# Kernel tuning notes

Hardware: AMD Instinct MI355X
Metric: run time of the kernel (lower is better)

The kernel has to match this reference:

```python
import jax, jax.numpy as jnp
import numpy as np

K = 3
THRESHOLD = 0.05
RADIUS = 0.1
MIN_CORR = 3
MAX_CORR = 1500
N_ITER = 5
EPS = 1e-5
P, N = 1024, 128


def setup_inputs() -> dict:
    key = jax.random.key(0)
    k1, k2, k3, k4, k5 = jax.random.split(key, 5)
    # local knn patches: small spatial extent so matching_radius=0.1 is meaningful
    ref_knn_points = jax.random.normal(k1, (P, N, 3), jnp.float32) * 0.05
    src_knn_points = jax.random.normal(k2, (P, N, 3), jnp.float32) * 0.05
    ref_knn_masks = jax.random.uniform(k3, (P, N)) > 0.1
    src_knn_masks = jax.random.uniform(k4, (P, N)) > 0.1
    matching_score_map = jax.random.normal(k5, (P, N, N), jnp.float32)
    return {
        'ref_knn_points': ref_knn_points,
        'src_knn_points': src_knn_points,
        'ref_knn_masks': ref_knn_masks,
        'src_knn_masks': src_knn_masks,
        'matching_score_map': matching_score_map,
    }


def _kabsch(H, src_c, ref_c, bad):
    # guard degenerate (all-zero-weight) problems with a fixed full-rank H
    safe = jnp.diag(jnp.asarray([3.0, 2.0, 1.0], H.dtype))
    H = jnp.where(bad[..., None, None], safe, H)
    U, S, Vt = jnp.linalg.svd(H)
    V = jnp.swapaxes(Vt, -1, -2)
    Ut = jnp.swapaxes(U, -1, -2)
    det = jnp.linalg.det(V @ Ut)
    D = jnp.zeros_like(H).at[..., 0, 0].set(1.0).at[..., 1, 1].set(1.0).at[..., 2, 2].set(det)
    R = V @ D @ Ut
    t = ref_c - jnp.einsum('...cd,...d->...c', R, src_c)
    T = jnp.zeros(H.shape[:-2] + (4, 4), H.dtype)
    return T.at[..., :3, :3].set(R).at[..., :3, 3].set(t).at[..., 3, 3].set(1.0)


def pair_procrustes(src, ref, w):
    # src, ref: (..., M, 3); w: (..., M)
    tot = jnp.sum(w, -1, keepdims=True)
    wn = w / (tot + EPS)
    src_c = jnp.einsum('...m,...mc->...c', wn, src)
    ref_c = jnp.einsum('...m,...mc->...c', wn, ref)
    H = jnp.einsum('...mc,...m,...md->...cd', src - src_c[..., None, :], wn, ref - ref_c[..., None, :])
    return _kabsch(H, src_c, ref_c, tot[..., 0] < EPS)


def grid_procrustes(src, ref, W):
    # per-proposal weighted Procrustes over the full (ref_i, src_j) pair grid;
    # identical math to gathering nonzero pairs since zero-weight pairs drop out
    tot = jnp.sum(W, (1, 2))  # (P,)
    Wn = W / (tot[:, None, None] + EPS)
    ref_c = jnp.einsum('pij,pic->pc', Wn, ref)
    src_c = jnp.einsum('pij,pjc->pc', Wn, src)
    H = jnp.einsum('pjc,pij,pid->pcd', src - src_c[:, None], Wn, ref - ref_c[:, None])
    return _kabsch(H, src_c, ref_c, tot < EPS)


def _forward(ref_knn_points, src_knn_points, ref_knn_masks, src_knn_masks, matching_score_map):
    Pn, Nn, _ = matching_score_map.shape
    sm = jnp.exp(matching_score_map)
    corr_mask = ref_knn_masks[:, :, None] & src_knn_masks[:, None, :]

    pidx = jnp.arange(Pn)[:, None, None]
    lidx = jnp.arange(Nn)[None, :, None]
    # topk over src dim -> ref_score_map
    ref_ts, ref_ti = jax.lax.top_k(sm, K)
    ref_score_map = jnp.zeros_like(sm).at[pidx, lidx, ref_ti].set(ref_ts)
    # topk over ref dim -> src_score_map (via transpose)
    smT = jnp.swapaxes(sm, 1, 2)
    src_ts, src_ti = jax.lax.top_k(smT, K)
    src_score_map = jnp.swapaxes(jnp.zeros_like(smT).at[pidx, lidx, src_ti].set(src_ts), 1, 2)

    ref_corr = (ref_score_map > THRESHOLD) & corr_mask
    src_corr = (src_score_map > THRESHOLD) & corr_mask
    score_map = 0.5 * (ref_score_map + src_score_map)
    corr_map = ref_corr & src_corr

    # per-proposal Procrustes with pair-grid weights (zero weight = not a corr)
    W = jnp.where(corr_map, score_map, 0.0)
    counts = jnp.sum(corr_map, (1, 2))
    valid = counts >= MIN_CORR
    transforms = grid_procrustes(src_knn_points, ref_knn_points, W)  # (P,4,4)

    # global capped correspondence pool (top MAX_CORR by score)
    flat = jnp.where(corr_map, score_map, -1.0).reshape(-1)
    top_scores, top_flat = jax.lax.top_k(flat, MAX_CORR)
    p = top_flat // (Nn * Nn)
    rem = top_flat % (Nn * Nn)
    i = rem // Nn
    j = rem % Nn
    real = top_scores > 0.0  # padded slots if fewer than MAX_CORR corrs
    corr_scores = jnp.where(real, top_scores, 0.0)
    ref_pts = ref_knn_points[p, i]   # (M,3)
    src_pts = src_knn_points[p, j]   # (M,3)
    # padded candidates pushed far away so they are never inliers
    src_eval = src_pts + jnp.where(real, 0.0, 1e6)[:, None]

    # evaluate every proposal transform on the capped pool, pick max-inlier
    aligned = jnp.einsum('pcd,md->pmc', transforms[:, :3, :3], src_eval) + transforms[:, None, :3, 3]
    d2 = jnp.sum((ref_pts[None] - aligned) ** 2, -1)  # (P,M)
    inliers = d2 < RADIUS ** 2
    icount = jnp.where(valid, jnp.sum(inliers, 1), -1)
    best = jnp.argmax(icount)

    cur = corr_scores * inliers[best].astype(corr_scores.dtype)
    T = pair_procrustes(src_pts, ref_pts, cur)
    for _ in range(N_ITER - 1):
        al = src_eval @ T[:3, :3].T + T[:3, 3]
        d2 = jnp.sum((ref_pts - al) ** 2, -1)
        cur = corr_scores * (d2 < RADIUS ** 2).astype(corr_scores.dtype)
        T = pair_procrustes(src_pts, ref_pts, cur)

    return ref_pts, src_pts, corr_scores, T


def reference(ref_knn_points, src_knn_points, ref_knn_masks, src_knn_masks, matching_score_map):
    return _forward(ref_knn_points, src_knn_points, ref_knn_masks, src_knn_masks, matching_score_map)
```

## Files before the change

kernel.cpp:

```cpp
#include <hip/hip_runtime.h>
#include <math.h>

#define PP    1024
#define NPT   128
#define NN2   16384
#define THRESH 0.05f
#define MAXC  1500
#define EPSD  1e-5
#define RRD   (0.1*0.1)
#define NEGF  -3.0e38f
#define MAXCPB 384
#define SELCAP 4096u

#define OFF_CCNT  0
#define OFF_ICNT  4096
#define OFF_TRANS 8192
#define OFF_POOL  106496
#define OFF_HDR   166496
#define OFF_SEL   166560
#define OFF_PHIST 199328
#define OFF_CLIST 1247904

__device__ inline void top3_upd(float v, float& a, float& b, float& c) {
  float m1 = fminf(a, v);
  a = fmaxf(a, v);
  float m2 = fminf(b, m1);
  b = fmaxf(b, m1);
  c = fmaxf(c, m2);
}
__device__ inline void merge3(float& a, float& b, float& c, float x0, float x1, float x2) {
  float z0 = fmaxf(a, x0);
  float z1 = fmaxf(fminf(a, x0), fmaxf(b, x1));
  float z2 = fmaxf(fmaxf(c, x2), fmaxf(fminf(b, x0), fminf(a, x1)));
  a = z0; b = z1; c = z2;
}

__device__ inline unsigned enc_f(float v) {
  unsigned b = __float_as_uint(v);
  return (b & 0x80000000u) ? ~b : (b | 0x80000000u);
}
__device__ inline float dec_f(unsigned enc) {
  unsigned b = (enc & 0x80000000u) ? (enc ^ 0x80000000u) : ~enc;
  return __uint_as_float(b);
}

__device__ inline void jacobi4(double A[4][4], double V[4][4]) {
  for (int i = 0; i < 4; ++i)
    for (int j = 0; j < 4; ++j) V[i][j] = (i == j) ? 1.0 : 0.0;
  const int PI_[6] = {0, 0, 0, 1, 1, 2};
  const int QI_[6] = {1, 2, 3, 2, 3, 3};
  for (int sweep = 0; sweep < 30; ++sweep) {
    double off = fabs(A[0][1]) + fabs(A[0][2]) + fabs(A[0][3]) +
                 fabs(A[1][2]) + fabs(A[1][3]) + fabs(A[2][3]);
    double dia = fabs(A[0][0]) + fabs(A[1][1]) + fabs(A[2][2]) + fabs(A[3][3]);
    if (off <= 1e-15 * (dia + 1e-300)) break;
#pragma unroll
    for (int r = 0; r < 6; ++r) {
      int p = PI_[r], q = QI_[r];
      double apq = A[p][q];
      if (fabs(apq) <= 1e-18 * (fabs(A[p][p]) + fabs(A[q][q]) + 1e-300)) continue;
      double theta = (A[q][q] - A[p][p]) / (2.0 * apq);
      double t = ((theta >= 0.0) ? 1.0 : -1.0) / (fabs(theta) + sqrt(1.0 + theta * theta));
      double c = 1.0 / sqrt(1.0 + t * t);
      double s = t * c;
#pragma unroll
      for (int k = 0; k < 4; ++k) {
        double akp = A[k][p], akq = A[k][q];
        A[k][p] = c * akp - s * akq;
        A[k][q] = s * akp + c * akq;
      }
#pragma unroll
      for (int k = 0; k < 4; ++k) {
        double apk = A[p][k], aqk = A[q][k];
        A[p][k] = c * apk - s * aqk;
        A[q][k] = s * apk + c * aqk;
      }
#pragma unroll
      for (int k = 0; k < 4; ++k) {
        double vkp = V[k][p], vkq = V[k][q];
        V[k][p] = c * vkp - s * vkq;
        V[k][q] = s * vkp + c * vkq;
      }
    }
  }
}

__device__ inline void kabsch_from_sums(double tot, const double* sr, const double* ss,
                                        const double* m9, double* T12) {
  double den = tot + EPSD;
  double rc[3], sc[3];
  for (int c = 0; c < 3; ++c) { rc[c] = sr[c] / den; sc[c] = ss[c] / den; }
  double sb = tot / den;
  double H[3][3];
  for (int c = 0; c < 3; ++c)
    for (int d = 0; d < 3; ++d)
      H[c][d] = m9[c * 3 + d] / den - (2.0 - sb) * sc[c] * rc[d];
  if (tot < EPSD) {
    H[0][0] = 3.0; H[0][1] = 0.0; H[0][2] = 0.0;
    H[1][0] = 0.0; H[1][1] = 2.0; H[1][2] = 0.0;
    H[2][0] = 0.0; H[2][1] = 0.0; H[2][2] = 1.0;
  }
  double Sxx = H[0][0], Sxy = H[0][1], Sxz = H[0][2];
  double Syx = H[1][0], Syy = H[1][1], Syz = H[1][2];
  double Szx = H[2][0], Szy = H[2][1], Szz = H[2][2];
  double A[4][4] = {
    {Sxx + Syy + Szz, Syz - Szy,        Szx - Sxz,         Sxy - Syx},
    {Syz - Szy,       Sxx - Syy - Szz,  Sxy + Syx,         Szx + Sxz},
    {Szx - Sxz,       Sxy + Syx,       -Sxx + Syy - Szz,   Syz + Szy},
    {Sxy - Syx,       Szx + Sxz,        Syz + Szy,        -Sxx - Syy + Szz}};
  double V[4][4];
  jacobi4(A, V);
  int kb = 0; double ev = A[0][0];
  for (int i = 1; i < 4; ++i) if (A[i][i] > ev) { ev = A[i][i]; kb = i; }
  double q0 = V[0][kb], qx = V[1][kb], qy = V[2][kb], qz = V[3][kb];
  double nrm = sqrt(q0 * q0 + qx * qx + qy * qy + qz * qz);
  if (nrm < 1e-300) { q0 = 1.0; qx = qy = qz = 0.0; nrm = 1.0; }
  q0 /= nrm; qx /= nrm; qy /= nrm; qz /= nrm;
  double R[3][3];
  R[0][0] = q0*q0 + qx*qx - qy*qy - qz*qz; R[0][1] = 2.0*(qx*qy - q0*qz); R[0][2] = 2.0*(qx*qz + q0*qy);
  R[1][0] = 2.0*(qx*qy + q0*qz); R[1][1] = q0*q0 - qx*qx + qy*qy - qz*qz; R[1][2] = 2.0*(qy*qz - q0*qx);
  R[2][0] = 2.0*(qx*qz - q0*qy); R[2][1] = 2.0*(qy*qz + q0*qx); R[2][2] = q0*q0 - qx*qx - qy*qy + qz*qz;
  for (int c = 0; c < 3; ++c)
    for (int d = 0; d < 3; ++d) T12[c * 3 + d] = R[c][d];
  for (int c = 0; c < 3; ++c)
    T12[9 + c] = rc[c] - (R[c][0] * sc[0] + R[c][1] * sc[1] + R[c][2] * sc[2]);
}

__global__ __launch_bounds__(256, 2) void k_fused(
    const float* __restrict__ scores, const void* __restrict__ mref,
    const void* __restrict__ msrc, unsigned* __restrict__ ccnt,
    unsigned long long* __restrict__ clist) {
  const int p = blockIdx.x;
  const int tid = threadIdx.x;
  __shared__ float tile[128 * 132];
  __shared__ float colpart[2][NPT][3];
  __shared__ float rthr[NPT], cthr[NPT];
  __shared__ unsigned char lmr[NPT];
  __shared__ unsigned lcnt;
  __shared__ unsigned masku8_s;
  if (tid == 0) lcnt = 0;
  if (tid < 64) {
    unsigned v = (tid < 32) ? ((const unsigned*)mref)[p * 32 + tid]
                            : ((const unsigned*)msrc)[p * 32 + (tid - 32)];
    unsigned long long any = __ballot(v > 1u);
    if (tid == 0) masku8_s = any ? 1u : 0u;
  }
  {
    const float4* S4 = (const float4*)(scores + (size_t)p * NN2);
    float4 vv[16];
#pragma unroll
    for (int s = 0; s < 16; ++s)
      vv[s] = S4[s * 256 + tid];
#pragma unroll
    for (int s = 0; s < 16; ++s) {
      int flat = (s * 256 + tid) * 4;
      int r = flat >> 7, c = flat & 127;
      *(float4*)&tile[r * 132 + c] = vv[s];
    }
  }
  __syncthreads();
  const unsigned maskU8 = masku8_s;
  if (tid < NPT)
    lmr[tid] = maskU8 ? (((const unsigned char*)mref)[p * NPT + tid] != 0)
                      : (((const int*)mref)[p * NPT + tid] != 0);
  const int col = tid & 127;
  const int half = tid >> 7;
  const bool msj = maskU8 ? (((const unsigned char*)msrc)[p * NPT + col] != 0)
                          : (((const int*)msrc)[p * NPT + col] != 0);
  for (int rb = 0; rb < 4; ++rb) {
    int r = rb * 32 + (tid >> 3);
    int o = tid & 7;
    float a = NEGF, b = NEGF, c = NEGF;
    const float4* tr = (const float4*)&tile[r * 132 + o * 16];
#pragma unroll
    for (int k = 0; k < 4; ++k) {
      float4 q = tr[k];
      top3_upd(q.x, a, b, c); top3_upd(q.y, a, b, c);
      top3_upd(q.z, a, b, c); top3_upd(q.w, a, b, c);
    }
#pragma unroll
    for (int m = 1; m < 8; m <<= 1) {
      float pa = __shfl_xor(a, m, 64), pb = __shfl_xor(b, m, 64), pc = __shfl_xor(c, m, 64);
      merge3(a, b, c, pa, pb, pc);
    }
    if (o == 0) rthr[r] = c;
  }
  {
    float a = NEGF, b = NEGF, c = NEGF;
    const float* tc = tile + (half * 64) * 132 + col;
#pragma unroll 8
    for (int r = 0; r < 64; ++r)
      top3_upd(tc[r * 132], a, b, c);
    colpart[half][col][0] = a; colpart[half][col][1] = b; colpart[half][col][2] = c;
  }
  __syncthreads();
  if (tid < NPT) {
    float a = colpart[0][tid][0], b = colpart[0][tid][1], c = colpart[0][tid][2];
    merge3(a, b, c, colpart[1][tid][0], colpart[1][tid][1], colpart[1][tid][2]);
    cthr[tid] = c;
  }
  __syncthreads();
  {
    const float cth = cthr[col];
    const float* tc = tile + (half * 64) * 132 + col;
#pragma unroll 4
    for (int it = 0; it < 64; ++it) {
      float v = tc[it * 132];
      int i = half * 64 + it;
      if (msj && v >= cth && v >= rthr[i] && lmr[i] && (expf(v) > THRESH)) {
        unsigned pos = atomicAdd(&lcnt, 1u);
        if (pos < MAXCPB) {
          unsigned long long key =
              (((unsigned long long)(~enc_f(v))) << 32) |
              (unsigned long long)(unsigned)(p * NN2 + i * NPT + col);
          clist[(size_t)p * MAXCPB + pos] = key;
        }
      }
    }
  }
  __syncthreads();
  if (tid == 0) ccnt[p] = (lcnt < MAXCPB) ? lcnt : MAXCPB;
}

__global__ __launch_bounds__(256) void k_hist(
    const unsigned* __restrict__ ccnt, const unsigned long long* __restrict__ clist,
    unsigned* __restrict__ phist) {
  __shared__ unsigned lh[4096];
  const int b = blockIdx.x, tid = threadIdx.x;
  for (int i = tid; i < 4096; i += 256) lh[i] = 0;
  __syncthreads();
  for (int q = 0; q < 16; ++q) {
    const int p = b * 16 + q;
    const unsigned cnt = min(ccnt[p], (unsigned)MAXCPB);
    const unsigned long long* my = clist + (size_t)p * MAXCPB;
    for (unsigned t = tid; t < cnt; t += 256)
      atomicAdd(&lh[(unsigned)(my[t] >> 52)], 1u);
  }
  __syncthreads();
  for (int i = tid; i < 4096; i += 256) phist[b * 4096 + i] = lh[i];
}

__global__ __launch_bounds__(1024) void k_cut(const unsigned* __restrict__ phist,
                                              unsigned* __restrict__ hdr) {
  __shared__ unsigned s[1024];
  __shared__ unsigned cb_s;
  const int tid = threadIdx.x;
  if (tid == 0) cb_s = 4095u;
  uint4 acc = make_uint4(0, 0, 0, 0);
  const uint4* ph4 = (const uint4*)phist;
#pragma unroll 4
  for (int b = 0; b < 64; ++b) {
    uint4 h = ph4[b * 1024 + tid];
    acc.x += h.x; acc.y += h.y; acc.z += h.z; acc.w += h.w;
  }
  s[tid] = acc.x + acc.y + acc.z + acc.w;
  __syncthreads();
  for (int off = 1; off < 1024; off <<= 1) {
    unsigned v = s[tid];
    unsigned a = (tid >= off) ? s[tid - off] : 0u;
    __syncthreads();
    s[tid] = v + a;
    __syncthreads();
  }
  {
    unsigned pre = (tid > 0) ? s[tid - 1] : 0u;
    unsigned tot4 = acc.x + acc.y + acc.z + acc.w;
    if (pre < MAXC && pre + tot4 >= MAXC) {
      unsigned c0 = pre + acc.x, c1 = c0 + acc.y, c2 = c1 + acc.z;
      cb_s = (c0 >= MAXC) ? tid * 4 : (c1 >= MAXC) ? tid * 4 + 1
           : (c2 >= MAXC) ? tid * 4 + 2 : tid * 4 + 3;
    }
  }
  __syncthreads();
  if (tid == 0) {
    hdr[0] = s[1023];
    hdr[1] = 0u;
    hdr[2] = cb_s;
  }
}

__global__ __launch_bounds__(256) void k_gather(
    const unsigned* __restrict__ ccnt, const unsigned long long* __restrict__ clist,
    unsigned* __restrict__ hdr, unsigned long long* __restrict__ sel) {
  const int b = blockIdx.x, tid = threadIdx.x, lane = tid & 63;
  const unsigned cut = hdr[2];
  for (int q = 0; q < 16; ++q) {
    const int p = b * 16 + q;
    const unsigned cnt = min(ccnt[p], (unsigned)MAXCPB);
    const unsigned long long* my = clist + (size_t)p * MAXCPB;
    for (unsigned t0 = 0; t0 < cnt; t0 += 256) {
      unsigned t = t0 + tid;
      unsigned long long key = 0;
      bool take = false;
      if (t < cnt) {
        key = my[t];
        take = ((unsigned)(key >> 52)) <= cut;
      }
      unsigned long long mb = __ballot(take);
      if (mb) {
        int leader = __ffsll((unsigned long long)mb) - 1;
        unsigned base = 0;
        if (lane == leader) base = atomicAdd(&hdr[1], (unsigned)__popcll(mb));
        base = __shfl(base, leader, 64);
        if (take) {
          unsigned pos = base + (unsigned)__popcll(mb & ((1ull << lane) - 1ull));
          if (pos < SELCAP) sel[pos] = key;
        }
      }
    }
  }
}

__global__ __launch_bounds__(1024) void k_sortout(
    const unsigned long long* __restrict__ sel, const unsigned* __restrict__ hdr,
    const float* __restrict__ refp, const float* __restrict__ srcp,
    float* __restrict__ pool, float* __restrict__ out) {
  __shared__ unsigned long long keys[4096];
  const int tid = threadIdx.x;
  const unsigned sc = min(hdr[1], SELCAP);
  for (unsigned t = tid; t < 4096u; t += 1024)
    keys[t] = (t < sc) ? sel[t] : 0xFFFFFFFFFFFFFFFFull;
  __syncthreads();
  for (unsigned k = 2; k <= 4096; k <<= 1) {
    for (unsigned j = k >> 1; j; j >>= 1) {
      for (unsigned t = tid; t < 4096; t += 1024) {
        unsigned ixj = t ^ j;
        if (ixj > t) {
          unsigned long long A = keys[t], B = keys[ixj];
          bool up = ((t & k) == 0);
          if (up ? (A > B) : (A < B)) { keys[t] = B; keys[ixj] = A; }
        }
      }
      __syncthreads();
    }
  }
  const unsigned stotal = hdr[0];
  const unsigned nreal = (stotal < MAXC) ? stotal : MAXC;
  for (int mm = tid; mm < MAXC; mm += 1024) {
    unsigned flat; float score; bool real = ((unsigned)mm < nreal);
    if (real) {
      unsigned long long key = keys[mm];
      flat = (unsigned)(key & 0xFFFFFFFFull);
      score = expf(dec_f(~(unsigned)(key >> 32)));
    } else {
      flat = (unsigned)mm;
      score = 0.f;
    }
    unsigned p = flat >> 14, rem = flat & 16383u, i = rem >> 7, j = rem & 127u;
    float rx = refp[((size_t)p * NPT + i) * 3 + 0];
    float ry = refp[((size_t)p * NPT + i) * 3 + 1];
    float rz = refp[((size_t)p * NPT + i) * 3 + 2];
    float sx = srcp[((size_t)p * NPT + j) * 3 + 0];
    float sy = srcp[((size_t)p * NPT + j) * 3 + 1];
    float sz = srcp[((size_t)p * NPT + j) * 3 + 2];
    out[mm * 3 + 0] = rx; out[mm * 3 + 1] = ry; out[mm * 3 + 2] = rz;
    out[4500 + mm * 3 + 0] = sx; out[4500 + mm * 3 + 1] = sy; out[4500 + mm * 3 + 2] = sz;
    out[9000 + mm] = score;
    pool[mm * 3 + 0] = rx; pool[mm * 3 + 1] = ry; pool[mm * 3 + 2] = rz;
    pool[4500 + mm * 3 + 0] = sx; pool[4500 + mm * 3 + 1] = sy; pool[4500 + mm * 3 + 2] = sz;
    float pad = real ? 0.f : 1e6f;
    pool[9000 + mm * 3 + 0] = sx + pad;
    pool[9000 + mm * 3 + 1] = sy + pad;
    pool[9000 + mm * 3 + 2] = sz + pad;
    pool[13500 + mm] = score;
  }
}

__global__ __launch_bounds__(256) void k_evalT(
    const unsigned* __restrict__ ccnt, const unsigned long long* __restrict__ clist,
    const float* __restrict__ refp, const float* __restrict__ srcp,
    const float* __restrict__ pool, double* __restrict__ trans,
    int* __restrict__ icount) {
  const int p = blockIdx.x, tid = threadIdx.x, lane = tid & 63;
  __shared__ double red[4][16];
  __shared__ double Ts[12];
  __shared__ int redc[4];
  const unsigned cnt = min(ccnt[p], (unsigned)MAXCPB);
  double tot = 0, sr0 = 0, sr1 = 0, sr2 = 0, ss0 = 0, ss1 = 0, ss2 = 0;
  double m00 = 0, m01 = 0, m02 = 0, m10 = 0, m11 = 0, m12 = 0, m20 = 0, m21 = 0, m22 = 0;
  for (unsigned t = tid; t < cnt; t += 256) {
    unsigned long long key = clist[(size_t)p * MAXCPB + t];
    unsigned flat = (unsigned)(key & 0xFFFFFFFFull);
    unsigned rem = flat & 16383u, i = rem >> 7, j = rem & 127u;
    double w = (double)expf(dec_f(~(unsigned)(key >> 32)));
    double rx = refp[((size_t)p * NPT + i) * 3 + 0];
    double ry = refp[((size_t)p * NPT + i) * 3 + 1];
    double rz = refp[((size_t)p * NPT + i) * 3 + 2];
    double sx = srcp[((size_t)p * NPT + j) * 3 + 0];
    double sy = srcp[((size_t)p * NPT + j) * 3 + 1];
    double sz = srcp[((size_t)p * NPT + j) * 3 + 2];
    tot += w;
    sr0 += w * rx; sr1 += w * ry; sr2 += w * rz;
    ss0 += w * sx; ss1 += w * sy; ss2 += w * sz;
    double wsx = w * sx, wsy = w * sy, wsz = w * sz;
    m00 += wsx * rx; m01 += wsx * ry; m02 += wsx * rz;
    m10 += wsy * rx; m11 += wsy * ry; m12 += wsy * rz;
    m20 += wsz * rx; m21 += wsz * ry; m22 += wsz * rz;
  }
  double vals[16] = {tot, sr0, sr1, sr2, ss0, ss1, ss2,
                     m00, m01, m02, m10, m11, m12, m20, m21, m22};
#pragma unroll
  for (int k = 0; k < 16; ++k) {
    double x = vals[k];
    for (int o = 32; o; o >>= 1) x += __shfl_down(x, o, 64);
    if (lane == 0) red[tid >> 6][k] = x;
  }
  __syncthreads();
  if (tid == 0) {
    double s16[16];
    for (int k = 0; k < 16; ++k)
      s16[k] = red[0][k] + red[1][k] + red[2][k] + red[3][k];
    kabsch_from_sums(s16[0], s16 + 1, s16 + 4, s16 + 7, Ts);
    for (int k = 0; k < 12; ++k) trans[p * 12 + k] = Ts[k];
  }
  __syncthreads();
  double R00 = Ts[0], R01 = Ts[1], R02 = Ts[2], R10 = Ts[3], R11 = Ts[4], R12 = Ts[5];
  double R20 = Ts[6], R21 = Ts[7], R22 = Ts[8], t0 = Ts[9], t1 = Ts[10], t2 = Ts[11];
  const float* pr = pool;
  const float* pe = pool + 9000;
  int c = 0;
  for (int mm = tid; mm < MAXC; mm += 256) {
    double ex = pe[mm * 3], ey = pe[mm * 3 + 1], ez = pe[mm * 3 + 2];
    double ax = R00 * ex + R01 * ey + R02 * ez + t0;
    double ay = R10 * ex + R11 * ey + R12 * ez + t1;
    double az = R20 * ex + R21 * ey + R22 * ez + t2;
    double dx = pr[mm * 3] - ax, dy = pr[mm * 3 + 1] - ay, dz = pr[mm * 3 + 2] - az;
    if (dx * dx + dy * dy + dz * dz < RRD) ++c;
  }
  for (int o = 32; o; o >>= 1) c += __shfl_down(c, o, 64);
  if (lane == 0) redc[tid >> 6] = c;
  __syncthreads();
  if (tid == 0) {
    int tc = redc[0] + redc[1] + redc[2] + redc[3];
    icount[p] = (cnt >= 3u) ? tc : -1;
  }
}

__global__ __launch_bounds__(256, 1) void k_refine(const double* __restrict__ trans,
                                                   const int* __restrict__ icount,
                                                   const float* __restrict__ pool,
                                                   float* __restrict__ out) {
  const int tid = threadIdx.x, lane = tid & 63;
  __shared__ int rc_[256], ri_[256];
  __shared__ double red[4][16];
  __shared__ double T[12];
  int bc = -2147483647, bi = 0;
  for (int idx = tid; idx < PP; idx += 256) {
    int c = icount[idx];
    if (c > bc) { bc = c; bi = idx; }
  }
  rc_[tid] = bc; ri_[tid] = bi;
  __syncthreads();
  for (int s = 128; s; s >>= 1) {
    if (tid < s) {
      int c2 = rc_[tid + s], i2 = ri_[tid + s];
      if (c2 > rc_[tid] || (c2 == rc_[tid] && i2 < ri_[tid])) { rc_[tid] = c2; ri_[tid] = i2; }
    }
    __syncthreads();
  }
  if (tid == 0) {
    int best = ri_[0];
    for (int k = 0; k < 12; ++k) T[k] = trans[best * 12 + k];
  }
  __syncthreads();
  const float* pr = pool;
  const float* ps = pool + 4500;
  const float* pe = pool + 9000;
  const float* pw = pool + 13500;
  for (int iter = 0; iter < 5; ++iter) {
    double R00 = T[0], R01 = T[1], R02 = T[2], R10 = T[3], R11 = T[4], R12 = T[5];
    double R20 = T[6], R21 = T[7], R22 = T[8], t0 = T[9], t1 = T[10], t2 = T[11];
    double tot = 0, sr0 = 0, sr1 = 0, sr2 = 0, ss0 = 0, ss1 = 0, ss2 = 0;
    double m00 = 0, m01 = 0, m02 = 0, m10 = 0, m11 = 0, m12 = 0, m20 = 0, m21 = 0, m22 = 0;
    for (int mm = tid; mm < MAXC; mm += 256) {
      double ex = pe[mm * 3], ey = pe[mm * 3 + 1], ez = pe[mm * 3 + 2];
      double ax = R00 * ex + R01 * ey + R02 * ez + t0;
      double ay = R10 * ex + R11 * ey + R12 * ez + t1;
      double az = R20 * ex + R21 * ey + R22 * ez + t2;
      double rx = pr[mm * 3], ry = pr[mm * 3 + 1], rz = pr[mm * 3 + 2];
      double dx = rx - ax, dy = ry - ay, dz = rz - az;
      if (dx * dx + dy * dy + dz * dz < RRD) {
        double w = (double)pw[mm];
        double sx = ps[mm * 3], sy = ps[mm * 3 + 1], sz = ps[mm * 3 + 2];
        tot += w;
        sr0 += w * rx; sr1 += w * ry; sr2 += w * rz;
        ss0 += w * sx; ss1 += w * sy; ss2 += w * sz;
        double wsx = w * sx, wsy = w * sy, wsz = w * sz;
        m00 += wsx * rx; m01 += wsx * ry; m02 += wsx * rz;
        m10 += wsy * rx; m11 += wsy * ry; m12 += wsy * rz;
        m20 += wsz * rx; m21 += wsz * ry; m22 += wsz * rz;
      }
    }
    double vals[16] = {tot, sr0, sr1, sr2, ss0, ss1, ss2,
                       m00, m01, m02, m10, m11, m12, m20, m21, m22};
#pragma unroll
    for (int k = 0; k < 16; ++k) {
      double x = vals[k];
      for (int o = 32; o; o >>= 1) x += __shfl_down(x, o, 64);
      if (lane == 0) red[tid >> 6][k] = x;
    }
    __syncthreads();
    if (tid == 0) {
      double s16[16];
      for (int k = 0; k < 16; ++k)
        s16[k] = red[0][k] + red[1][k] + red[2][k] + red[3][k];
      kabsch_from_sums(s16[0], s16 + 1, s16 + 4, s16 + 7, T);
    }
    __syncthreads();
  }
  if (tid == 0) {
    out[10500 + 0]  = (float)T[0]; out[10500 + 1]  = (float)T[1];
    out[10500 + 2]  = (float)T[2]; out[10500 + 3]  = (float)T[9];
    out[10500 + 4]  = (float)T[3]; out[10500 + 5]  = (float)T[4];
    out[10500 + 6]  = (float)T[5]; out[10500 + 7]  = (float)T[10];
    out[10500 + 8]  = (float)T[6]; out[10500 + 9]  = (float)T[7];
    out[10500 + 10] = (float)T[8]; out[10500 + 11] = (float)T[11];
    out[10500 + 12] = 0.f; out[10500 + 13] = 0.f;
    out[10500 + 14] = 0.f; out[10500 + 15] = 1.f;
  }
}

extern "C" void kernel_launch(void* const* d_in, const int* in_sizes, int n_in,
                              void* d_out, int out_size, void* d_ws, size_t ws_size,
                              hipStream_t stream) {
  const float* refp = (const float*)d_in[0];
  const float* srcp = (const float*)d_in[1];
  const void* mref = d_in[2];
  const void* msrc = d_in[3];
  const float* scores = (const float*)d_in[4];
  float* out = (float*)d_out;
  char* ws = (char*)d_ws;
  unsigned* ccnt = (unsigned*)(ws + OFF_CCNT);
  int* icount = (int*)(ws + OFF_ICNT);
  double* trans = (double*)(ws + OFF_TRANS);
  float* pool = (float*)(ws + OFF_POOL);
  unsigned* hdr = (unsigned*)(ws + OFF_HDR);
  unsigned long long* sel = (unsigned long long*)(ws + OFF_SEL);
  unsigned* phist = (unsigned*)(ws + OFF_PHIST);
  unsigned long long* clist = (unsigned long long*)(ws + OFF_CLIST);

  k_fused<<<PP, 256, 0, stream>>>(scores, mref, msrc, ccnt, clist);
  k_hist<<<64, 256, 0, stream>>>(ccnt, clist, phist);
  k_cut<<<1, 1024, 0, stream>>>(phist, hdr);
  k_gather<<<64, 256, 0, stream>>>(ccnt, clist, hdr, sel);
  k_sortout<<<1, 1024, 0, stream>>>(sel, hdr, refp, srcp, pool, out);
  k_evalT<<<PP, 256, 0, stream>>>(ccnt, clist, refp, srcp, pool, trans, icount);
  k_refine<<<1, 256, 0, stream>>>(trans, icount, pool, out);
}
```

Measured before the change: 367.0 us.

## Replace Jacobi eigensolver with Newton on quaternion characteristic polynomial

The Kabsch step now finds the largest eigenvalue of Horn's 4x4 quaternion matrix by Newton iteration on its closed-form characteristic polynomial, started from a Gershgorin bound. The eigenvector comes from the adjugate row with the largest cofactor. The cyclic Jacobi solver is kept only as a fallback for near-degenerate cases, and its loops are no longer unrolled to reduce code size and register pressure. This targets the serial double-precision cost of the per-proposal rotation solve, at the risk of lower accuracy when eigenvalues are nearly repeated.

```diff
diff --git a/kernel.cpp b/kernel.cpp
--- a/kernel.cpp
+++ b/kernel.cpp
@@ -53,8 +53,7 @@
     double off = fabs(A[0][1]) + fabs(A[0][2]) + fabs(A[0][3]) +
                  fabs(A[1][2]) + fabs(A[1][3]) + fabs(A[2][3]);
     double dia = fabs(A[0][0]) + fabs(A[1][1]) + fabs(A[2][2]) + fabs(A[3][3]);
-    if (off <= 1e-15 * (dia + 1e-300)) break;
-#pragma unroll
+    if (off <= 1e-14 * (dia + 1e-300)) break;
     for (int r = 0; r < 6; ++r) {
       int p = PI_[r], q = QI_[r];
       double apq = A[p][q];
@@ -63,19 +62,16 @@
       double t = ((theta >= 0.0) ? 1.0 : -1.0) / (fabs(theta) + sqrt(1.0 + theta * theta));
       double c = 1.0 / sqrt(1.0 + t * t);
       double s = t * c;
-#pragma unroll
       for (int k = 0; k < 4; ++k) {
         double akp = A[k][p], akq = A[k][q];
         A[k][p] = c * akp - s * akq;
         A[k][q] = s * akp + c * akq;
       }
-#pragma unroll
       for (int k = 0; k < 4; ++k) {
         double apk = A[p][k], aqk = A[q][k];
         A[p][k] = c * apk - s * aqk;
         A[q][k] = s * apk + c * aqk;
       }
-#pragma unroll
       for (int k = 0; k < 4; ++k) {
         double vkp = V[k][p], vkq = V[k][q];
         V[k][p] = c * vkp - s * vkq;
@@ -83,6 +79,19 @@
       }
     }
   }
+}
+
+__device__ inline double cof3(const double M[4][4], int rr, int cc) {
+  int ri[3], ci[3];
+  int n = 0;
+  for (int i = 0; i < 4; ++i) if (i != rr) ri[n++] = i;
+  n = 0;
+  for (int j = 0; j < 4; ++j) if (j != cc) ci[n++] = j;
+  double a = M[ri[0]][ci[0]], b = M[ri[0]][ci[1]], c = M[ri[0]][ci[2]];
+  double d = M[ri[1]][ci[0]], e = M[ri[1]][ci[1]], f = M[ri[1]][ci[2]];
+  double g = M[ri[2]][ci[0]], h = M[ri[2]][ci[1]], i2 = M[ri[2]][ci[2]];
+  double m = a * (e * i2 - f * h) - b * (d * i2 - f * g) + c * (d * h - e * g);
+  return (((rr + cc) & 1) ? -m : m);
 }
 
 __device__ inline void kabsch_from_sums(double tot, const double* sr, const double* ss,
@@ -103,19 +112,65 @@
   double Sxx = H[0][0], Sxy = H[0][1], Sxz = H[0][2];
   double Syx = H[1][0], Syy = H[1][1], Syz = H[1][2];
   double Szx = H[2][0], Szy = H[2][1], Szz = H[2][2];
-  double A[4][4] = {
+  double N[4][4] = {
     {Sxx + Syy + Szz, Syz - Szy,        Szx - Sxz,         Sxy - Syx},
     {Syz - Szy,       Sxx - Syy - Szz,  Sxy + Syx,         Szx + Sxz},
     {Szx - Sxz,       Sxy + Syx,       -Sxx + Syy - Szz,   Syz + Szy},
     {Sxy - Syx,       Szx + Sxz,        Syz + Szy,        -Sxx - Syy + Szz}};
-  double V[4][4];
-  jacobi4(A, V);
-  int kb = 0; double ev = A[0][0];
-  for (int i = 1; i < 4; ++i) if (A[i][i] > ev) { ev = A[i][i]; kb = i; }
-  double q0 = V[0][kb], qx = V[1][kb], qy = V[2][kb], qz = V[3][kb];
-  double nrm = sqrt(q0 * q0 + qx * qx + qy * qy + qz * qz);
-  if (nrm < 1e-300) { q0 = 1.0; qx = qy = qz = 0.0; nrm = 1.0; }
-  q0 /= nrm; qx /= nrm; qy /= nrm; qz /= nrm;
+  double fro2 = Sxx*Sxx + Sxy*Sxy + Sxz*Sxz + Syx*Syx + Syy*Syy + Syz*Syz +
+                Szx*Szx + Szy*Szy + Szz*Szz;
+  double c2 = -2.0 * fro2;
+  double c1 = -8.0 * (Sxx * (Syy * Szz - Syz * Szy) -
+                      Sxy * (Syx * Szz - Syz * Szx) +
+                      Sxz * (Syx * Szy - Syy * Szx));
+  double c0 = N[0][0] * cof3(N, 0, 0) + N[0][1] * cof3(N, 0, 1) +
+              N[0][2] * cof3(N, 0, 2) + N[0][3] * cof3(N, 0, 3);
+  double lam = -1e300;
+  for (int i = 0; i < 4; ++i) {
+    double r = N[i][i];
+    for (int j = 0; j < 4; ++j) if (j != i) r += fabs(N[i][j]);
+    lam = fmax(lam, r);
+  }
+  for (int it = 0; it < 100; ++it) {
+    double l2 = lam * lam;
+    double pv = ((l2 + c2) * lam + c1) * lam + c0;
+    double dp = (4.0 * l2 + 2.0 * c2) * lam + c1;
+    if (dp == 0.0) break;
+    double d = pv / dp;
+    lam -= d;
+    if (fabs(d) <= 1e-14 * fmax(fabs(lam), 1e-30)) break;
+  }
+  double K[4][4];
+  for (int i = 0; i < 4; ++i)
+    for (int j = 0; j < 4; ++j) K[i][j] = N[i][j];
+  for (int i = 0; i < 4; ++i) K[i][i] -= lam;
+  int jb = 0;
+  double bestd = -1.0;
+  for (int j = 0; j < 4; ++j) {
+    double dj = fabs(cof3(K, j, j));
+    if (dj > bestd) { bestd = dj; jb = j; }
+  }
+  double v[4];
+  for (int i = 0; i < 4; ++i) v[i] = cof3(K, jb, i);
+  double vn2 = v[0]*v[0] + v[1]*v[1] + v[2]*v[2] + v[3]*v[3];
+  double scl = sqrt(fro2) + fabs(lam) + 1e-300;
+  double thr = 1e-10 * scl * scl * scl;
+  double q0, qx, qy, qz;
+  if (vn2 > thr * thr) {
+    double inv = 1.0 / sqrt(vn2);
+    q0 = v[0] * inv; qx = v[1] * inv; qy = v[2] * inv; qz = v[3] * inv;
+  } else {
+    double A[4][4], V[4][4];
+    for (int i = 0; i < 4; ++i)
+      for (int j = 0; j < 4; ++j) A[i][j] = N[i][j];
+    jacobi4(A, V);
+    int kb = 0; double ev = A[0][0];
+    for (int i = 1; i < 4; ++i) if (A[i][i] > ev) { ev = A[i][i]; kb = i; }
+    double w0 = V[0][kb], w1 = V[1][kb], w2 = V[2][kb], w3 = V[3][kb];
+    double nr = sqrt(w0*w0 + w1*w1 + w2*w2 + w3*w3);
+    if (nr < 1e-300) { w0 = 1.0; w1 = w2 = w3 = 0.0; nr = 1.0; }
+    q0 = w0 / nr; qx = w1 / nr; qy = w2 / nr; qz = w3 / nr;
+  }
   double R[3][3];
   R[0][0] = q0*q0 + qx*qx - qy*qy - qz*qz; R[0][1] = 2.0*(qx*qy - q0*qz); R[0][2] = 2.0*(qx*qz + q0*qy);
   R[1][0] = 2.0*(qx*qy + q0*qz); R[1][1] = q0*q0 - qx*qx + qy*qy - qz*qz; R[1][2] = 2.0*(qy*qz - q0*qx);
```

Result: faster. 325.2 us (-11.4%).
